# Optimization experiments

Hardware: AMD Instinct MI355X
Metric: run time of the kernel (lower is better)

The kernel has to match this reference:

```python
import jax, jax.numpy as jnp
import numpy as np

B, D_IN, D_OUT, S = 8192, 1024, 4096, 64
C = D_OUT // S          # chunk size per seed = 64
H = 2 * C               # blueprint hidden = 128


def setup_inputs() -> dict:
    key = jax.random.key(0)
    ks = jax.random.split(key, 9)
    sc = lambda *shape: 1.0 / np.sqrt(shape[-1] if len(shape) > 1 else 1.0)
    x = jax.random.normal(ks[0], (B, D_IN), jnp.float32)
    Wb = jax.random.normal(ks[1], (D_OUT, D_IN), jnp.float32) * (1.0 / np.sqrt(D_IN))
    bb = jax.random.normal(ks[2], (D_OUT,), jnp.float32) * 0.01
    W1 = jax.random.normal(ks[3], (S, C, H), jnp.float32) * (1.0 / np.sqrt(C))
    b1 = jax.random.normal(ks[4], (S, H), jnp.float32) * 0.01
    W2 = jax.random.normal(ks[5], (S, H, C), jnp.float32) * (1.0 / np.sqrt(H))
    b2 = jax.random.normal(ks[6], (S, C), jnp.float32) * 0.01
    alpha = jax.random.uniform(ks[7], (S,), jnp.float32)
    active = jax.random.randint(ks[8], (S,), 0, 2) > 0  # bool mask of active seeds
    return {"x": x, "Wb": Wb, "bb": bb, "W1": W1, "b1": b1,
            "W2": W2, "b2": b2, "alpha": alpha, "active": active}


def reference(x, Wb, bb, W1, b1, W2, b2, alpha, active):
    # base layer: Linear(D_IN -> D_OUT)
    base = x @ Wb.T + bb                       # [B, D_OUT]
    y = base.reshape(B, S, C)                  # chunked view: [B, S, C]
    # per-seed blueprint MLP: Linear(C, 2C) -> ReLU -> Linear(2C, C), grouped over seeds
    h = jax.nn.relu(jnp.einsum('bsc,sch->bsh', y, W1) + b1)   # [B, S, H]
    bp = jnp.einsum('bsh,shc->bsc', h, W2) + b2               # [B, S, C]
    # alpha-blend only for active seeds; inactive seeds pass chunk through
    a = (alpha * active.astype(alpha.dtype))[None, :, None]    # [1, S, 1]
    out = (1.0 - a) * y + a * bp               # [B, S, C]
    return out.reshape(B, D_OUT)
```

## Files before the change

### kernel.cpp

```cpp
#include <hip/hip_runtime.h>
#include <stdint.h>

typedef unsigned short u16;
typedef __bf16 bf16x8 __attribute__((ext_vector_type(8)));
typedef unsigned short u16x8 __attribute__((ext_vector_type(8)));
typedef u16x8 u16x8_ma __attribute__((may_alias));
typedef unsigned short u16x4 __attribute__((ext_vector_type(4)));
typedef float f32x4 __attribute__((ext_vector_type(4)));

#define DIN   1024
#define DOUT  4096
#define BM    128
#define BN    128
#define BK    64

__device__ __forceinline__ u16 f2bf(float f) {
  unsigned u = __float_as_uint(f);
  u += 0x7fffu + ((u >> 16) & 1u);
  return (u16)(u >> 16);
}
__device__ __forceinline__ bf16x8 ldfrag(const u16* p) {
  union { u16x8 u; bf16x8 b; } cv;
  cv.u = *(const u16x8_ma*)p;
  return cv.b;
}
__device__ __forceinline__ f32x4 mfma16(bf16x8 a, bf16x8 b, f32x4 c) {
  return __builtin_amdgcn_mfma_f32_16x16x32_bf16(a, b, c, 0, 0, 0);
}
__device__ __forceinline__ void gload_lds16(const u16* g, u16* l) {
  __builtin_amdgcn_global_load_lds(
      (const __attribute__((address_space(1))) void*)g,
      (__attribute__((address_space(3))) void*)l, 16, 0, 0);
}
__device__ __forceinline__ void wave_lds_fence() {
  __asm__ __volatile__("s_waitcnt lgkmcnt(0)" ::: "memory");
}

__global__ void prep_all(const float* __restrict__ X, const float* __restrict__ Wb,
                         const float* __restrict__ W1, const float* __restrict__ W2,
                         u16* __restrict__ Xb, u16* __restrict__ Wbb,
                         u16* __restrict__ W1T, u16* __restrict__ W2T) {
  __shared__ u16 tile[8192];
  const int b = blockIdx.x;
  const int t = threadIdx.x;

  if (b < 3072) {
    const float* src; u16* dst; int n4, i, stride;
    if (b < 2048) { src = X;  dst = Xb;  n4 = (8192 * 1024) / 4; i = b * 256 + t;          stride = 2048 * 256; }
    else          { src = Wb; dst = Wbb; n4 = (4096 * 1024) / 4; i = (b - 2048) * 256 + t; stride = 1024 * 256; }
    for (; i < n4; i += stride) {
      f32x4 v = ((const f32x4*)src)[i];
      u16x4 o;
      o.x = f2bf(v.x); o.y = f2bf(v.y); o.z = f2bf(v.z); o.w = f2bf(v.w);
      ((u16x4*)dst)[i] = o;
    }
    return;
  }

  const int s = b - 3072;
  const float* w1 = W1 + s * 8192;
  u16* w1t = W1T + s * 8192;
  for (int i = t; i < 8192; i += 256) tile[i] = f2bf(w1[i]);
  __syncthreads();
  for (int i = t; i < 8192; i += 256) {
    int h = i >> 6, c = i & 63;
    w1t[i] = tile[c * 128 + h];
  }
  __syncthreads();

  const float* w2 = W2 + s * 8192;
  u16* w2t = W2T + s * 8192;
  for (int i = t; i < 8192; i += 256) tile[i] = f2bf(w2[i]);
  __syncthreads();
  for (int i = t; i < 8192; i += 256) {
    int c = i >> 7, h = i & 127;
    w2t[i] = tile[h * 64 + c];
  }
}

__global__ __launch_bounds__(256, 2) void kasmina_fused(
    const u16* __restrict__ X,   const u16* __restrict__ Wb,
    const float* __restrict__ bb,  const float* __restrict__ b1,
    const float* __restrict__ b2,  const float* __restrict__ alpha,
    const int* __restrict__ active,
    const u16* __restrict__ W1T, const u16* __restrict__ W2T,
    float* __restrict__ out)
{
  __shared__ u16 lds[18432];

  const int t = threadIdx.x;
  const int w = t >> 6, l = t & 63;
  const int wm = w >> 1, wn = w & 1;
  const int lane15 = l & 15, quad = l >> 4;
  const int bn0 = blockIdx.x * BN;
  const int bm0 = blockIdx.y * BM;

  f32x4 acc[4][4];
#pragma unroll
  for (int mt = 0; mt < 4; ++mt)
#pragma unroll
    for (int nt = 0; nt < 4; ++nt)
      acc[mt][nt] = (f32x4){0.f, 0.f, 0.f, 0.f};

  const int srow = l >> 3;
  const int scol = ((l & 7) ^ srow) << 3;
  const u16* xg = X  + (size_t)(bm0 + srow) * DIN + scol;
  const u16* wg = Wb + (size_t)(bn0 + srow) * DIN + scol;

  const int xr = lane15 & 7;
  const int oswz = (quad ^ xr) << 3;
  const u16* Ab = &lds[(wm * 64 + lane15) * 64];
  const u16* Bb = &lds[8192 + (wn * 64 + lane15) * 64];

  for (int kt = 0; kt < DIN / BK; ++kt) {
    const int k0 = kt * BK;
#pragma unroll
    for (int i = 0; i < 4; ++i) {
      const int q = i * 4 + w;
      gload_lds16(xg + (size_t)(q * 8) * DIN + k0, &lds[q * 512]);
      gload_lds16(wg + (size_t)(q * 8) * DIN + k0, &lds[8192 + q * 512]);
    }
    __syncthreads();
#pragma unroll
    for (int ks = 0; ks < 2; ++ks) {
      const int o = oswz ^ (ks << 5);
      bf16x8 af[4], bfx[4];
#pragma unroll
      for (int mt = 0; mt < 4; ++mt) af[mt] = ldfrag(Ab + mt * 1024 + o);
#pragma unroll
      for (int nt = 0; nt < 4; ++nt) bfx[nt] = ldfrag(Bb + nt * 1024 + o);
#pragma unroll
      for (int mt = 0; mt < 4; ++mt)
#pragma unroll
        for (int nt = 0; nt < 4; ++nt)
          acc[mt][nt] = mfma16(af[mt], bfx[nt], acc[mt][nt]);
    }
    __syncthreads();
  }

  const int sidx = blockIdx.x * 2 + wn;
  const int act = active[sidx];
  float bbv[4];
#pragma unroll
  for (int nt = 0; nt < 4; ++nt) bbv[nt] = bb[sidx * 64 + nt * 16 + lane15];

  const size_t orow0 = (size_t)(bm0 + wm * 64);

  if (!act) {
#pragma unroll
    for (int mt = 0; mt < 4; ++mt)
#pragma unroll
      for (int nt = 0; nt < 4; ++nt) {
        f32x4 yv = acc[mt][nt];
        const int col = sidx * 64 + nt * 16 + lane15;
#pragma unroll
        for (int r = 0; r < 4; ++r) {
          const size_t row = orow0 + mt * 16 + quad * 4 + r;
          out[row * DOUT + col] = yv[r] + bbv[nt];
        }
      }
    return;
  }

  const float aval = alpha[sidx];

  u16* Yw = &lds[w * 4608];
  u16* Hw = Yw + 2304;

#pragma unroll
  for (int mh = 0; mh < 2; ++mh) {
#pragma unroll
    for (int mt = 0; mt < 2; ++mt)
#pragma unroll
      for (int nt = 0; nt < 4; ++nt) {
        f32x4 v = acc[mh * 2 + mt][nt];
        const int col = nt * 16 + lane15;
#pragma unroll
        for (int r = 0; r < 4; ++r)
          Yw[(mt * 16 + quad * 4 + r) * 72 + col] = f2bf(v[r] + bbv[nt]);
      }
    wave_lds_fence();

    f32x4 bp[2][4];
#pragma unroll
    for (int nt = 0; nt < 4; ++nt) {
      const float b2v = b2[sidx * 64 + nt * 16 + lane15];
      const f32x4 tv = (f32x4){b2v, b2v, b2v, b2v};
      bp[0][nt] = tv; bp[1][nt] = tv;
    }

#pragma unroll 1
    for (int hh = 0; hh < 2; ++hh) {
      f32x4 hc[2][4];
#pragma unroll
      for (int nt = 0; nt < 4; ++nt) {
        const float b1v = b1[sidx * 128 + hh * 64 + nt * 16 + lane15];
        const f32x4 tv = (f32x4){b1v, b1v, b1v, b1v};
        hc[0][nt] = tv; hc[1][nt] = tv;
      }
      const u16* w1b = W1T + sidx * 8192 + (hh * 64 + lane15) * 64 + quad * 8;
#pragma unroll
      for (int ks = 0; ks < 2; ++ks) {
        bf16x8 af0 = ldfrag(Yw + lane15 * 72 + ks * 32 + quad * 8);
        bf16x8 af1 = ldfrag(Yw + (16 + lane15) * 72 + ks * 32 + quad * 8);
#pragma unroll
        for (int nt = 0; nt < 4; ++nt) {
          bf16x8 bfr = ldfrag(w1b + nt * 1024 + ks * 32);
          hc[0][nt] = mfma16(af0, bfr, hc[0][nt]);
          hc[1][nt] = mfma16(af1, bfr, hc[1][nt]);
        }
      }
#pragma unroll
      for (int mt = 0; mt < 2; ++mt)
#pragma unroll
        for (int nt = 0; nt < 4; ++nt) {
          f32x4 v = hc[mt][nt];
          const int col = nt * 16 + lane15;
#pragma unroll
          for (int r = 0; r < 4; ++r) {
            float hv = v[r] > 0.f ? v[r] : 0.f;
            Hw[(mt * 16 + quad * 4 + r) * 72 + col] = f2bf(hv);
          }
        }
      wave_lds_fence();
      const u16* w2b = W2T + sidx * 8192 + lane15 * 128 + hh * 64 + quad * 8;
#pragma unroll
      for (int ks = 0; ks < 2; ++ks) {
        bf16x8 af0 = ldfrag(Hw + lane15 * 72 + ks * 32 + quad * 8);
        bf16x8 af1 = ldfrag(Hw + (16 + lane15) * 72 + ks * 32 + quad * 8);
#pragma unroll
        for (int nt = 0; nt < 4; ++nt) {
          bf16x8 bfr = ldfrag(w2b + nt * 2048 + ks * 32);
          bp[0][nt] = mfma16(af0, bfr, bp[0][nt]);
          bp[1][nt] = mfma16(af1, bfr, bp[1][nt]);
        }
      }
      wave_lds_fence();
    }
#pragma unroll
    for (int mt = 0; mt < 2; ++mt)
#pragma unroll
      for (int nt = 0; nt < 4; ++nt) {
        f32x4 yv = acc[mh * 2 + mt][nt];
        f32x4 pv = bp[mt][nt];
        const int col = sidx * 64 + nt * 16 + lane15;
#pragma unroll
        for (int r = 0; r < 4; ++r) {
          const float y = yv[r] + bbv[nt];
          const float o = (1.0f - aval) * y + aval * pv[r];
          const size_t row = orow0 + mh * 32 + mt * 16 + quad * 4 + r;
          out[row * DOUT + col] = o;
        }
      }
    wave_lds_fence();
  }
}

extern "C" void kernel_launch(void* const* d_in, const int* in_sizes, int n_in,
                              void* d_out, int out_size, void* d_ws, size_t ws_size,
                              hipStream_t stream) {
  const float* X     = (const float*)d_in[0];
  const float* Wb    = (const float*)d_in[1];
  const float* bbp   = (const float*)d_in[2];
  const float* W1    = (const float*)d_in[3];
  const float* b1p   = (const float*)d_in[4];
  const float* W2    = (const float*)d_in[5];
  const float* b2p   = (const float*)d_in[6];
  const float* alpha = (const float*)d_in[7];
  const int*  active = (const int*)d_in[8];
  float* out = (float*)d_out;

  u16* W1T = (u16*)d_ws;
  u16* W2T = W1T + 524288;
  u16* Xb  = W1T + 1048576;
  u16* Wbb = W1T + 9437184;

  prep_all<<<3136, 256, 0, stream>>>(X, Wb, W1, W2, Xb, Wbb, W1T, W2T);
  kasmina_fused<<<dim3(32, 64), 256, 0, stream>>>(
      Xb, Wbb, bbp, b1p, b2p, alpha, active, W1T, W2T, out);
}
```

Before: 311.6 us.

## Enlarge GEMM tile to 256x256 with 8 waves and double-buffered LDS pipeline

Grows the block tile from 128x128 to 256x256 with 512 threads (8 waves, each owning 128x64), and double-buffers the LDS so global-to-LDS loads for step k+2 are issued while MFMAs run on the current buffer. Compute is split into phases separated by barriers, with s_setprio raised around the MFMA phases and explicit vmcnt waits. The aim is more reuse per loaded byte and hiding global-load latency. The cost is 128 KB of LDS per block, far more accumulator registers, more barriers, and a grid of only 512 blocks, which may leave few waves resident per CU.

```diff
diff --git a/kernel.cpp b/kernel.cpp
--- a/kernel.cpp
+++ b/kernel.cpp
@@ -10,8 +10,8 @@
 
 #define DIN   1024
 #define DOUT  4096
-#define BM    128
-#define BN    128
+#define BM    256
+#define BN    256
 #define BK    64
 
 __device__ __forceinline__ u16 f2bf(float f) {
@@ -78,7 +78,7 @@
   }
 }
 
-__global__ __launch_bounds__(256, 2) void kasmina_fused(
+__global__ __launch_bounds__(512, 2) void kasmina_fused(
     const u16* __restrict__ X,   const u16* __restrict__ Wb,
     const float* __restrict__ bb,  const float* __restrict__ b1,
     const float* __restrict__ b2,  const float* __restrict__ alpha,
@@ -86,69 +86,130 @@
     const u16* __restrict__ W1T, const u16* __restrict__ W2T,
     float* __restrict__ out)
 {
-  __shared__ u16 lds[18432];
+  __shared__ u16 lds[65536];
 
   const int t = threadIdx.x;
   const int w = t >> 6, l = t & 63;
-  const int wm = w >> 1, wn = w & 1;
+  const int wm = w >> 2, wn = w & 3;
   const int lane15 = l & 15, quad = l >> 4;
   const int bn0 = blockIdx.x * BN;
   const int bm0 = blockIdx.y * BM;
 
-  f32x4 acc[4][4];
-#pragma unroll
-  for (int mt = 0; mt < 4; ++mt)
+  f32x4 acc[8][4];
+#pragma unroll
+  for (int mt = 0; mt < 8; ++mt)
 #pragma unroll
     for (int nt = 0; nt < 4; ++nt)
       acc[mt][nt] = (f32x4){0.f, 0.f, 0.f, 0.f};
 
   const int srow = l >> 3;
   const int scol = ((l & 7) ^ srow) << 3;
-  const u16* xg = X  + (size_t)(bm0 + srow) * DIN + scol;
-  const u16* wg = Wb + (size_t)(bn0 + srow) * DIN + scol;
+  const int arow = wm * 128 + wn * 32;
+  const int brow = wn * 64 + wm * 32;
+  const u16* Ag = X  + (size_t)(bm0 + arow + srow) * DIN + scol;
+  const u16* Bg = Wb + (size_t)(bn0 + brow + srow) * DIN + scol;
+  u16* Albase = lds + arow * 64;
+  u16* Blbase = lds + 16384 + brow * 64;
 
   const int xr = lane15 & 7;
   const int oswz = (quad ^ xr) << 3;
-  const u16* Ab = &lds[(wm * 64 + lane15) * 64];
-  const u16* Bb = &lds[8192 + (wn * 64 + lane15) * 64];
-
-  for (int kt = 0; kt < DIN / BK; ++kt) {
-    const int k0 = kt * BK;
-#pragma unroll
-    for (int i = 0; i < 4; ++i) {
-      const int q = i * 4 + w;
-      gload_lds16(xg + (size_t)(q * 8) * DIN + k0, &lds[q * 512]);
-      gload_lds16(wg + (size_t)(q * 8) * DIN + k0, &lds[8192 + q * 512]);
-    }
-    __syncthreads();
-#pragma unroll
-    for (int ks = 0; ks < 2; ++ks) {
-      const int o = oswz ^ (ks << 5);
-      bf16x8 af[4], bfx[4];
-#pragma unroll
-      for (int mt = 0; mt < 4; ++mt) af[mt] = ldfrag(Ab + mt * 1024 + o);
-#pragma unroll
-      for (int nt = 0; nt < 4; ++nt) bfx[nt] = ldfrag(Bb + nt * 1024 + o);
-#pragma unroll
-      for (int mt = 0; mt < 4; ++mt)
-#pragma unroll
-        for (int nt = 0; nt < 4; ++nt)
-          acc[mt][nt] = mfma16(af[mt], bfx[nt], acc[mt][nt]);
-    }
-    __syncthreads();
-  }
-
-  const int sidx = blockIdx.x * 2 + wn;
+
+#pragma unroll
+  for (int c = 0; c < 4; ++c) {
+    gload_lds16(Ag + (size_t)(c * 8) * DIN + 0,  Albase + c * 512);
+    gload_lds16(Bg + (size_t)(c * 8) * DIN + 0,  Blbase + c * 512);
+  }
+#pragma unroll
+  for (int c = 0; c < 4; ++c) {
+    gload_lds16(Ag + (size_t)(c * 8) * DIN + 64, Albase + 32768 + c * 512);
+    gload_lds16(Bg + (size_t)(c * 8) * DIN + 64, Blbase + 32768 + c * 512);
+  }
+  __asm__ __volatile__("s_waitcnt vmcnt(8)" ::: "memory");
+  __builtin_amdgcn_s_barrier();
+
+#pragma unroll 1
+  for (int j = 0; j < 16; ++j) {
+    const int cur = j & 1;
+    const u16* Ab = lds + cur * 32768 + (wm * 128 + lane15) * 64;
+    const u16* Bb = lds + cur * 32768 + 16384 + (wn * 64 + lane15) * 64;
+
+    bf16x8 a0[8], b0[4], a1[8], b1f[4];
+#pragma unroll
+    for (int mt = 0; mt < 8; ++mt) a0[mt] = ldfrag(Ab + mt * 1024 + oswz);
+#pragma unroll
+    for (int nt = 0; nt < 4; ++nt) b0[nt] = ldfrag(Bb + nt * 1024 + oswz);
+    wave_lds_fence();
+    __builtin_amdgcn_s_barrier();
+    __builtin_amdgcn_s_setprio(1);
+#pragma unroll
+    for (int mt = 0; mt < 4; ++mt)
+#pragma unroll
+      for (int nt = 0; nt < 4; ++nt)
+        acc[mt][nt] = mfma16(a0[mt], b0[nt], acc[mt][nt]);
+    __builtin_amdgcn_s_setprio(0);
+    __builtin_amdgcn_s_barrier();
+
+#pragma unroll
+    for (int mt = 0; mt < 8; ++mt) a1[mt] = ldfrag(Ab + mt * 1024 + (oswz ^ 32));
+#pragma unroll
+    for (int nt = 0; nt < 4; ++nt) b1f[nt] = ldfrag(Bb + nt * 1024 + (oswz ^ 32));
+    wave_lds_fence();
+    __builtin_amdgcn_s_barrier();
+    __builtin_amdgcn_s_setprio(1);
+#pragma unroll
+    for (int mt = 4; mt < 8; ++mt)
+#pragma unroll
+      for (int nt = 0; nt < 4; ++nt)
+        acc[mt][nt] = mfma16(a0[mt], b0[nt], acc[mt][nt]);
+    __builtin_amdgcn_s_setprio(0);
+    __builtin_amdgcn_s_barrier();
+
+    if (j < 14) {
+      const int k0 = (j + 2) * 64;
+#pragma unroll
+      for (int c = 0; c < 4; ++c)
+        gload_lds16(Ag + (size_t)(c * 8) * DIN + k0, Albase + cur * 32768 + c * 512);
+    }
+    __builtin_amdgcn_s_barrier();
+    __builtin_amdgcn_s_setprio(1);
+#pragma unroll
+    for (int mt = 0; mt < 4; ++mt)
+#pragma unroll
+      for (int nt = 0; nt < 4; ++nt)
+        acc[mt][nt] = mfma16(a1[mt], b1f[nt], acc[mt][nt]);
+    __builtin_amdgcn_s_setprio(0);
+    __builtin_amdgcn_s_barrier();
+
+    if (j < 14) {
+      const int k0 = (j + 2) * 64;
+#pragma unroll
+      for (int c = 0; c < 4; ++c)
+        gload_lds16(Bg + (size_t)(c * 8) * DIN + k0, Blbase + cur * 32768 + c * 512);
+    }
+    if (j < 14)       { __asm__ __volatile__("s_waitcnt vmcnt(8)" ::: "memory"); }
+    else if (j == 14) { __asm__ __volatile__("s_waitcnt vmcnt(0)" ::: "memory"); }
+    __builtin_amdgcn_s_barrier();
+    __builtin_amdgcn_s_setprio(1);
+#pragma unroll
+    for (int mt = 4; mt < 8; ++mt)
+#pragma unroll
+      for (int nt = 0; nt < 4; ++nt)
+        acc[mt][nt] = mfma16(a1[mt], b1f[nt], acc[mt][nt]);
+    __builtin_amdgcn_s_setprio(0);
+    __builtin_amdgcn_s_barrier();
+  }
+
+  const int sidx = blockIdx.x * 4 + wn;
   const int act = active[sidx];
   float bbv[4];
 #pragma unroll
   for (int nt = 0; nt < 4; ++nt) bbv[nt] = bb[sidx * 64 + nt * 16 + lane15];
 
-  const size_t orow0 = (size_t)(bm0 + wm * 64);
+  const size_t orow0 = (size_t)(bm0 + wm * 128);
 
   if (!act) {
 #pragma unroll
-    for (int mt = 0; mt < 4; ++mt)
+    for (int mt = 0; mt < 8; ++mt)
 #pragma unroll
       for (int nt = 0; nt < 4; ++nt) {
         f32x4 yv = acc[mt][nt];
@@ -168,7 +229,7 @@
   u16* Hw = Yw + 2304;
 
 #pragma unroll
-  for (int mh = 0; mh < 2; ++mh) {
+  for (int mh = 0; mh < 4; ++mh) {
 #pragma unroll
     for (int mt = 0; mt < 2; ++mt)
 #pragma unroll
@@ -276,6 +337,6 @@
   u16* Wbb = W1T + 9437184;
 
   prep_all<<<3136, 256, 0, stream>>>(X, Wb, W1, W2, Xb, Wbb, W1T, W2T);
-  kasmina_fused<<<dim3(32, 64), 256, 0, stream>>>(
+  kasmina_fused<<<dim3(16, 32), 512, 0, stream>>>(
       Xb, Wbb, bbp, b1p, b2p, alpha, active, W1T, W2T, out);
 }
```

Result: faster. 302.5 us (-2.9%).

## Enlarge GEMM tile to 256x256 with 512 threads and 4-stage LDS pipeline

Applied to the files above, without the earlier changes.

Changes the fused GEMM main loop from 128x128x64 tiles with a single synchronous LDS buffer to 256x256x32 tiles using 8 waves and a four-deep ring of LDS buffers. Global-to-LDS loads for tile j+3 are issued while MFMAs on tile j run, split into two halves with s_setprio raised around the MFMA bursts. The aim is to hide global load latency and raise arithmetic intensity per block. In exchange it uses 128 KB of LDS and twice the accumulators per wave, which lowers occupancy; the grid also shrinks to 512 blocks, which may underfill the GPU's compute units.

```diff
diff --git a/kernel.cpp b/kernel.cpp
--- a/kernel.cpp
+++ b/kernel.cpp
@@ -10,9 +10,11 @@
 
 #define DIN   1024
 #define DOUT  4096
-#define BM    128
-#define BN    128
-#define BK    64
+#define BM    256
+#define BN    256
+#define BK    32
+#define NTILE 32
+#define BUFSZ 16384
 
 __device__ __forceinline__ u16 f2bf(float f) {
   unsigned u = __float_as_uint(f);
@@ -78,7 +80,7 @@
   }
 }
 
-__global__ __launch_bounds__(256, 2) void kasmina_fused(
+__global__ __launch_bounds__(512, 2) void kasmina_fused(
     const u16* __restrict__ X,   const u16* __restrict__ Wb,
     const float* __restrict__ bb,  const float* __restrict__ b1,
     const float* __restrict__ b2,  const float* __restrict__ alpha,
@@ -86,69 +88,101 @@
     const u16* __restrict__ W1T, const u16* __restrict__ W2T,
     float* __restrict__ out)
 {
-  __shared__ u16 lds[18432];
+  __shared__ u16 lds[65536];
 
   const int t = threadIdx.x;
   const int w = t >> 6, l = t & 63;
-  const int wm = w >> 1, wn = w & 1;
+  const int wm = w >> 2, wn = w & 3;
   const int lane15 = l & 15, quad = l >> 4;
   const int bn0 = blockIdx.x * BN;
   const int bm0 = blockIdx.y * BM;
 
-  f32x4 acc[4][4];
-#pragma unroll
-  for (int mt = 0; mt < 4; ++mt)
+  f32x4 acc[8][4];
+#pragma unroll
+  for (int mt = 0; mt < 8; ++mt)
 #pragma unroll
     for (int nt = 0; nt < 4; ++nt)
       acc[mt][nt] = (f32x4){0.f, 0.f, 0.f, 0.f};
 
-  const int srow = l >> 3;
-  const int scol = ((l & 7) ^ srow) << 3;
-  const u16* xg = X  + (size_t)(bm0 + srow) * DIN + scol;
-  const u16* wg = Wb + (size_t)(bn0 + srow) * DIN + scol;
-
-  const int xr = lane15 & 7;
-  const int oswz = (quad ^ xr) << 3;
-  const u16* Ab = &lds[(wm * 64 + lane15) * 64];
-  const u16* Bb = &lds[8192 + (wn * 64 + lane15) * 64];
-
-  for (int kt = 0; kt < DIN / BK; ++kt) {
-    const int k0 = kt * BK;
-#pragma unroll
-    for (int i = 0; i < 4; ++i) {
-      const int q = i * 4 + w;
-      gload_lds16(xg + (size_t)(q * 8) * DIN + k0, &lds[q * 512]);
-      gload_lds16(wg + (size_t)(q * 8) * DIN + k0, &lds[8192 + q * 512]);
-    }
-    __syncthreads();
-#pragma unroll
-    for (int ks = 0; ks < 2; ++ks) {
-      const int o = oswz ^ (ks << 5);
-      bf16x8 af[4], bfx[4];
-#pragma unroll
-      for (int mt = 0; mt < 4; ++mt) af[mt] = ldfrag(Ab + mt * 1024 + o);
-#pragma unroll
-      for (int nt = 0; nt < 4; ++nt) bfx[nt] = ldfrag(Bb + nt * 1024 + o);
-#pragma unroll
-      for (int mt = 0; mt < 4; ++mt)
-#pragma unroll
-        for (int nt = 0; nt < 4; ++nt)
-          acc[mt][nt] = mfma16(af[mt], bfx[nt], acc[mt][nt]);
-    }
-    __syncthreads();
-  }
-
-  const int sidx = blockIdx.x * 2 + wn;
+  const int rl = l >> 2;
+  const int cs = ((l & 3) ^ ((l >> 3) & 3)) << 3;
+  const u16* Ag = X  + (size_t)(bm0 + w * 16 + rl) * DIN + cs;
+  const u16* Bg = Wb + (size_t)(bn0 + w * 16 + rl) * DIN + cs;
+
+  const int swz = (quad ^ ((lane15 >> 1) & 3)) << 3;
+  const int aoff = (wm * 128 + lane15) * 32 + swz;
+  const int boff = 8192 + (wn * 64 + lane15) * 32 + swz;
+
+#pragma unroll
+  for (int tt = 0; tt < 3; ++tt) {
+    const int k0 = tt * BK;
+    u16* dst = &lds[tt * BUFSZ];
+    gload_lds16(Ag + k0,                    dst + w * 512);
+    gload_lds16(Ag + (size_t)128 * DIN + k0, dst + 4096 + w * 512);
+    gload_lds16(Bg + k0,                    dst + 8192 + w * 512);
+    gload_lds16(Bg + (size_t)128 * DIN + k0, dst + 12288 + w * 512);
+  }
+  __asm__ __volatile__("s_waitcnt vmcnt(8)" ::: "memory");
+  __builtin_amdgcn_s_barrier();
+
+#pragma unroll 1
+  for (int j = 0; j < NTILE; ++j) {
+    const u16* bufp = &lds[(j & 3) * BUFSZ];
+    const int stg = (j + 3) & 3;
+    const int k0n = (j + 3) * BK;
+
+    bf16x8 bfr[4], afr[4], afr2[4];
+#pragma unroll
+    for (int nt = 0; nt < 4; ++nt) bfr[nt] = ldfrag(bufp + boff + nt * 512);
+#pragma unroll
+    for (int mt = 0; mt < 4; ++mt) afr[mt] = ldfrag(bufp + aoff + mt * 512);
+    if (j < NTILE - 3) {
+      u16* dst = &lds[stg * BUFSZ];
+      gload_lds16(Ag + k0n,                     dst + w * 512);
+      gload_lds16(Ag + (size_t)128 * DIN + k0n, dst + 4096 + w * 512);
+    }
+    __builtin_amdgcn_s_barrier();
+    __builtin_amdgcn_s_setprio(1);
+#pragma unroll
+    for (int mt = 0; mt < 4; ++mt)
+#pragma unroll
+      for (int nt = 0; nt < 4; ++nt)
+        acc[mt][nt] = mfma16(afr[mt], bfr[nt], acc[mt][nt]);
+    __builtin_amdgcn_s_setprio(0);
+    __builtin_amdgcn_s_barrier();
+
+#pragma unroll
+    for (int mt = 0; mt < 4; ++mt) afr2[mt] = ldfrag(bufp + aoff + (mt + 4) * 512);
+    if (j < NTILE - 3) {
+      u16* dst = &lds[stg * BUFSZ];
+      gload_lds16(Bg + k0n,                     dst + 8192 + w * 512);
+      gload_lds16(Bg + (size_t)128 * DIN + k0n, dst + 12288 + w * 512);
+    }
+    if (j < NTILE - 3)       { __asm__ __volatile__("s_waitcnt vmcnt(8)" ::: "memory"); }
+    else if (j == NTILE - 3) { __asm__ __volatile__("s_waitcnt vmcnt(4)" ::: "memory"); }
+    else if (j == NTILE - 2) { __asm__ __volatile__("s_waitcnt vmcnt(0)" ::: "memory"); }
+    __builtin_amdgcn_s_barrier();
+    __builtin_amdgcn_s_setprio(1);
+#pragma unroll
+    for (int mt = 0; mt < 4; ++mt)
+#pragma unroll
+      for (int nt = 0; nt < 4; ++nt)
+        acc[mt + 4][nt] = mfma16(afr2[mt], bfr[nt], acc[mt + 4][nt]);
+    __builtin_amdgcn_s_setprio(0);
+    __builtin_amdgcn_s_barrier();
+  }
+
+  const int sidx = blockIdx.x * 4 + wn;
   const int act = active[sidx];
   float bbv[4];
 #pragma unroll
   for (int nt = 0; nt < 4; ++nt) bbv[nt] = bb[sidx * 64 + nt * 16 + lane15];
 
-  const size_t orow0 = (size_t)(bm0 + wm * 64);
+  const size_t orow0 = (size_t)(bm0 + wm * 128);
 
   if (!act) {
 #pragma unroll
-    for (int mt = 0; mt < 4; ++mt)
+    for (int mt = 0; mt < 8; ++mt)
 #pragma unroll
       for (int nt = 0; nt < 4; ++nt) {
         f32x4 yv = acc[mt][nt];
@@ -168,7 +202,7 @@
   u16* Hw = Yw + 2304;
 
 #pragma unroll
-  for (int mh = 0; mh < 2; ++mh) {
+  for (int mh = 0; mh < 4; ++mh) {
 #pragma unroll
     for (int mt = 0; mt < 2; ++mt)
 #pragma unroll
@@ -276,6 +310,6 @@
   u16* Wbb = W1T + 9437184;
 
   prep_all<<<3136, 256, 0, stream>>>(X, Wb, W1, W2, Xb, Wbb, W1T, W2T);
-  kasmina_fused<<<dim3(32, 64), 256, 0, stream>>>(
+  kasmina_fused<<<dim3(16, 32), 512, 0, stream>>>(
       Xb, Wbb, bbp, b1p, b2p, alpha, active, W1T, W2T, out);
 }
```

Result: faster. 297.4 us (-4.5%).

## Triple-buffer GEMM main loop with async LDS loads and XCD-aware block remap

Applied to the files above, without the earlier changes.

Replaces the synchronous load-then-compute loop with a three-stage LDS ring (BK reduced to 32), issuing global-to-LDS loads two tiles ahead and using vmcnt waits plus a single barrier per iteration. It also remaps workgroup IDs so consecutive blocks on each XCD share tiles for L2 reuse, and raises wave priority around the MFMA burst. The aim is to hide global memory latency behind matrix math and cut barrier stalls. The cost is more LDS per block (48KB), which may reduce occupancy, and relying on manual waitcnt ordering.

```diff
diff --git a/kernel.cpp b/kernel.cpp
--- a/kernel.cpp
+++ b/kernel.cpp
@@ -12,7 +12,9 @@
 #define DOUT  4096
 #define BM    128
 #define BN    128
-#define BK    64
+#define BK    32
+#define NTILE 32
+#define BUFSZ 8192
 
 __device__ __forceinline__ u16 f2bf(float f) {
   unsigned u = __float_as_uint(f);
@@ -86,14 +88,17 @@
     const u16* __restrict__ W1T, const u16* __restrict__ W2T,
     float* __restrict__ out)
 {
-  __shared__ u16 lds[18432];
+  __shared__ u16 lds[24576];
 
   const int t = threadIdx.x;
   const int w = t >> 6, l = t & 63;
   const int wm = w >> 1, wn = w & 1;
   const int lane15 = l & 15, quad = l >> 4;
-  const int bn0 = blockIdx.x * BN;
-  const int bm0 = blockIdx.y * BM;
+
+  const int wgid = blockIdx.y * 32 + blockIdx.x;
+  const int s = (wgid & 7) * 256 + (wgid >> 3);
+  const int bn0 = (s & 31) * BN;
+  const int bm0 = (s >> 5) * BM;
 
   f32x4 acc[4][4];
 #pragma unroll
@@ -102,43 +107,56 @@
     for (int nt = 0; nt < 4; ++nt)
       acc[mt][nt] = (f32x4){0.f, 0.f, 0.f, 0.f};
 
-  const int srow = l >> 3;
-  const int scol = ((l & 7) ^ srow) << 3;
-  const u16* xg = X  + (size_t)(bm0 + srow) * DIN + scol;
-  const u16* wg = Wb + (size_t)(bn0 + srow) * DIN + scol;
-
-  const int xr = lane15 & 7;
-  const int oswz = (quad ^ xr) << 3;
-  const u16* Ab = &lds[(wm * 64 + lane15) * 64];
-  const u16* Bb = &lds[8192 + (wn * 64 + lane15) * 64];
-
-  for (int kt = 0; kt < DIN / BK; ++kt) {
-    const int k0 = kt * BK;
-#pragma unroll
-    for (int i = 0; i < 4; ++i) {
-      const int q = i * 4 + w;
-      gload_lds16(xg + (size_t)(q * 8) * DIN + k0, &lds[q * 512]);
-      gload_lds16(wg + (size_t)(q * 8) * DIN + k0, &lds[8192 + q * 512]);
-    }
-    __syncthreads();
-#pragma unroll
-    for (int ks = 0; ks < 2; ++ks) {
-      const int o = oswz ^ (ks << 5);
-      bf16x8 af[4], bfx[4];
-#pragma unroll
-      for (int mt = 0; mt < 4; ++mt) af[mt] = ldfrag(Ab + mt * 1024 + o);
-#pragma unroll
-      for (int nt = 0; nt < 4; ++nt) bfx[nt] = ldfrag(Bb + nt * 1024 + o);
-#pragma unroll
-      for (int mt = 0; mt < 4; ++mt)
-#pragma unroll
-        for (int nt = 0; nt < 4; ++nt)
-          acc[mt][nt] = mfma16(af[mt], bfx[nt], acc[mt][nt]);
-    }
-    __syncthreads();
-  }
-
-  const int sidx = blockIdx.x * 2 + wn;
+  const int rl = l >> 2;
+  const int cs = ((l & 3) ^ ((l >> 3) & 3)) << 3;
+  const u16* Ag = X  + (size_t)(bm0 + w * 32 + rl) * DIN + cs;
+  const u16* Bg = Wb + (size_t)(bn0 + w * 32 + rl) * DIN + cs;
+
+  const int swz = (quad ^ ((lane15 >> 1) & 3)) << 3;
+  const int aoff = (wm * 64 + lane15) * 32 + swz;
+  const int boff = 4096 + (wn * 64 + lane15) * 32 + swz;
+
+#define VM4 __asm__ __volatile__("s_waitcnt vmcnt(4)" ::: "memory")
+#define VM0 __asm__ __volatile__("s_waitcnt vmcnt(0)" ::: "memory")
+
+#define STAGE(J) do {                                                    \
+    const int kk_ = (J) * BK;                                            \
+    u16* dst_ = &lds[((J) % 3) * BUFSZ];                                 \
+    gload_lds16(Ag + kk_,            dst_ +        w * 1024);            \
+    gload_lds16(Ag + 16 * DIN + kk_, dst_ +  512 + w * 1024);            \
+    gload_lds16(Bg + kk_,            dst_ + 4096 + w * 1024);            \
+    gload_lds16(Bg + 16 * DIN + kk_, dst_ + 4608 + w * 1024);            \
+  } while (0)
+
+  STAGE(0); STAGE(1);
+  VM4;
+  __builtin_amdgcn_s_barrier();
+
+#pragma unroll 1
+  for (int j = 0; j < NTILE; ++j) {
+    const u16* bufp = &lds[(j % 3) * BUFSZ];
+    bf16x8 afr[4], bfr[4];
+#pragma unroll
+    for (int nt = 0; nt < 4; ++nt) bfr[nt] = ldfrag(bufp + boff + nt * 512);
+#pragma unroll
+    for (int mt = 0; mt < 4; ++mt) afr[mt] = ldfrag(bufp + aoff + mt * 512);
+    if (j < NTILE - 2) {
+      STAGE(j + 2);
+      VM4;
+    } else if (j == NTILE - 2) {
+      VM0;
+    }
+    __builtin_amdgcn_s_setprio(1);
+#pragma unroll
+    for (int mt = 0; mt < 4; ++mt)
+#pragma unroll
+      for (int nt = 0; nt < 4; ++nt)
+        acc[mt][nt] = mfma16(afr[mt], bfr[nt], acc[mt][nt]);
+    __builtin_amdgcn_s_setprio(0);
+    __builtin_amdgcn_s_barrier();
+  }
+
+  const int sidx = (s & 31) * 2 + wn;
   const int act = active[sidx];
   float bbv[4];
 #pragma unroll
```

Measured after the change: 313.6 us. No clear change (+0.6%).
